# Kernel tuning notes

Measured on AMD Instinct MI355X. Metric: run time of the kernel, lower is better.

The kernel has to match this reference:

```python
import jax, jax.numpy as jnp
import numpy as np

ALPHA = 300.0  # attractor strength (exp variant: exp(-alpha*|dx|^gamma)*dx, gamma=2)


def setup_inputs() -> dict:
    key = jax.random.key(0)
    k0, k1, k2, k3 = jax.random.split(key, 4)
    n, c, h, w = 4, 256, 128, 128
    mlp_dim, n_attractors, n_bins = 128, 16, 64
    x = jax.random.normal(k0, (n, c, h, w), jnp.float32)
    b_prev = jax.random.uniform(k1, (n, n_bins, h, w), jnp.float32)  # bin centers
    w1 = jax.random.normal(k2, (mlp_dim, c), jnp.float32) * 0.02
    b1 = jnp.zeros((mlp_dim,), jnp.float32)
    w2 = jax.random.normal(k3, (n_attractors, mlp_dim), jnp.float32) * 0.02
    b2 = jnp.zeros((n_attractors,), jnp.float32)
    return {"x": x, "b_prev": b_prev, "w1": w1, "b1": b1, "w2": w2, "b2": b2}


def reference(x, b_prev, w1, b1, w2, b2):
    # 1x1 conv MLP head: Conv2d(c->mlp) -> ReLU -> Conv2d(mlp->n_attractors) -> Softplus
    hfeat = jax.nn.relu(jnp.einsum('nchw,oc->nohw', x, w1) + b1[None, :, None, None])
    A = jax.nn.softplus(jnp.einsum('nchw,oc->nohw', hfeat, w2) + b2[None, :, None, None])
    # b_prev interpolated to (h, w) == identity here (same spatial size)
    b_centers = b_prev
    # dx: [n, n_attractors, n_bins, h, w]
    dx = A[:, :, None, :, :] - b_centers[:, None, :, :, :]
    # exp attractor with gamma=2: exp(-alpha*dx^2) * dx, summed over attractors ('sum' kind)
    delta_c = jnp.sum(jnp.exp(-ALPHA * dx * dx) * dx, axis=1)
    b_new_centers = b_centers + delta_c
    return (b_new_centers, b_new_centers)
```

## Files before the change

kernel.cpp:

```cpp
#include <hip/hip_runtime.h>
#include <hip/hip_bf16.h>
#include <stdint.h>


#define HW 16384
#define ALPHA 300.0f

typedef short bf16x8_t __attribute__((ext_vector_type(8)));
typedef float f32x4_t __attribute__((ext_vector_type(4)));

__device__ __forceinline__ unsigned short f2bf(float f) {
  unsigned int u = __builtin_bit_cast(unsigned int, f);
  u += 0x7fffu + ((u >> 16) & 1u);
  return (unsigned short)(u >> 16);
}
__device__ __forceinline__ unsigned int pack2(float a, float b) {
  return (unsigned int)f2bf(a) | ((unsigned int)f2bf(b) << 16);
}

__global__ void zoed_prep(const float* __restrict__ w1,
                          const float* __restrict__ w2,
                          unsigned short* __restrict__ blob) {
  int i = blockIdx.x * 256 + threadIdx.x;
  if (i < 32768) {
    int o = i >> 8, c = i & 255;
    blob[(c >> 5) * 4096 + o * 32 + (c & 31)] = f2bf(w1[i]);
  } else {
    int i2 = i - 32768;
    int a = i2 >> 7, o = i2 & 127;
    blob[32768 + (o >> 5) * 512 + a * 32 + (o & 31)] = f2bf(w2[i2]);
  }
}

__global__ __launch_bounds__(256, 4) void zoed_mlp(
    const float* __restrict__ x, const float* __restrict__ b1,
    const float* __restrict__ b2, const unsigned short* __restrict__ wblob,
    float* __restrict__ A) {
  __shared__ __align__(16) char smem[16384];
  const int t = threadIdx.x;
  const int lane = t & 63;
  const int l15 = lane & 15;
  const int quad = lane >> 4;
  const int wv = t >> 6;
  char* hb = smem + wv * 4096;

  const int wid = blockIdx.x * 4 + wv;
  const int px0 = wid * 16;
  const int n = px0 >> 14;
  const int p = px0 & 16383;

  const float* xb = x + (size_t)(n * 256 + quad * 8) * HW + p + l15;
  float xr[8][8];
#pragma unroll
  for (int kc = 0; kc < 8; kc++)
#pragma unroll
    for (int j = 0; j < 8; j++) xr[kc][j] = xb[(size_t)(kc * 32 + j) * HW];

  f32x4_t acc[8];
#pragma unroll
  for (int m = 0; m < 8; m++) acc[m] = (f32x4_t){0.f, 0.f, 0.f, 0.f};

  const char* wb1 = (const char*)wblob + l15 * 64 + quad * 16;
#pragma unroll
  for (int kc = 0; kc < 8; kc++) {
    bf16x8_t bfrag;
    unsigned int* bu = (unsigned int*)&bfrag;
    bu[0] = pack2(xr[kc][0], xr[kc][1]);
    bu[1] = pack2(xr[kc][2], xr[kc][3]);
    bu[2] = pack2(xr[kc][4], xr[kc][5]);
    bu[3] = pack2(xr[kc][6], xr[kc][7]);
#pragma unroll
    for (int m = 0; m < 8; m++) {
      bf16x8_t af = *(const bf16x8_t*)(wb1 + kc * 8192 + m * 1024);
      acc[m] = __builtin_amdgcn_mfma_f32_16x16x32_bf16(af, bfrag, acc[m], 0, 0, 0);
    }
  }

#pragma unroll
  for (int m = 0; m < 8; m++) {
    f32x4_t b1v = *(const f32x4_t*)(b1 + m * 16 + quad * 4);
    f32x4_t h = acc[m] + b1v;
    h[0] = fmaxf(h[0], 0.f);
    h[1] = fmaxf(h[1], 0.f);
    h[2] = fmaxf(h[2], 0.f);
    h[3] = fmaxf(h[3], 0.f);
    int G = m * 2 + (quad >> 1);
    unsigned int* dst = (unsigned int*)(hb + l15 * 256 + ((G ^ (l15 & 3)) << 4) +
                                        (quad & 1) * 8);
    dst[0] = pack2(h[0], h[1]);
    dst[1] = pack2(h[2], h[3]);
  }

  f32x4_t acc2 = (f32x4_t){0.f, 0.f, 0.f, 0.f};
  const char* wb2 = (const char*)wblob + 65536 + l15 * 64 + quad * 16;
#pragma unroll
  for (int kc2 = 0; kc2 < 4; kc2++) {
    bf16x8_t a2 = *(const bf16x8_t*)(wb2 + kc2 * 1024);
    int G = kc2 * 4 + quad;
    bf16x8_t bh = *(const bf16x8_t*)(hb + l15 * 256 + ((G ^ (l15 & 3)) << 4));
    acc2 = __builtin_amdgcn_mfma_f32_16x16x32_bf16(a2, bh, acc2, 0, 0, 0);
  }
  f32x4_t b2v = *(const f32x4_t*)(b2 + quad * 4);
  float* Ab = A + (size_t)(n * 16 + quad * 4) * HW + p + l15;
#pragma unroll
  for (int r = 0; r < 4; r++) {
    float zz = acc2[r] + b2v[r];
    float sp = fmaxf(zz, 0.f) + log1pf(__expf(-fabsf(zz)));
    Ab[(size_t)r * HW] = sp;
  }
}

__global__ __launch_bounds__(256, 4) void zoed_attr(
    const float* __restrict__ bprev, const float* __restrict__ A,
    float* __restrict__ out) {
  const int t = threadIdx.x;
  const int blk = blockIdx.x;
  const int P = (blk & 255) * 256 + t;
  const int bg = blk >> 8;
  const int n = P >> 14;
  const int p = P & 16383;

  const float* Ab = A + (size_t)(n * 16) * HW + p;
  float Av[16];
#pragma unroll
  for (int a = 0; a < 16; a++) Av[a] = Ab[(size_t)a * HW];

  size_t obase = (size_t)(n * 64 + bg * 16) * HW + p;
  const float* bp = bprev + obase;
  float bpr[16];
#pragma unroll
  for (int b = 0; b < 16; b++) bpr[b] = bp[(size_t)b * HW];

  float* o1 = out + obase;
  float* o2 = out + (size_t)(4 * 64) * HW + obase;
#pragma unroll
  for (int b = 0; b < 16; b++) {
    float c = bpr[b];
    float d0 = 0.f, d1 = 0.f;
#pragma unroll
    for (int a = 0; a < 8; a++) {
      float dx = Av[a] - c;
      float e = __expf(dx * dx * -ALPHA);
      d0 = fmaf(e, dx, d0);
    }
#pragma unroll
    for (int a = 8; a < 16; a++) {
      float dx = Av[a] - c;
      float e = __expf(dx * dx * -ALPHA);
      d1 = fmaf(e, dx, d1);
    }
    float r = c + (d0 + d1);
    __builtin_nontemporal_store(r, o1 + (size_t)b * HW);
    __builtin_nontemporal_store(r, o2 + (size_t)b * HW);
  }
}

extern "C" void kernel_launch(void* const* d_in, const int* in_sizes, int n_in,
                              void* d_out, int out_size, void* d_ws,
                              size_t ws_size, hipStream_t stream) {
  const float* x = (const float*)d_in[0];
  const float* bprev = (const float*)d_in[1];
  const float* w1 = (const float*)d_in[2];
  const float* b1 = (const float*)d_in[3];
  const float* w2 = (const float*)d_in[4];
  const float* b2 = (const float*)d_in[5];
  float* outp = (float*)d_out;

  unsigned short* blob = (unsigned short*)d_ws;
  float* Abuf = (float*)((char*)d_ws + (1 << 20));

  zoed_prep<<<136, 256, 0, stream>>>(w1, w2, blob);
  zoed_mlp<<<1024, 256, 0, stream>>>(x, b1, b2, blob, Abuf);
  zoed_attr<<<1024, 256, 0, stream>>>(bprev, Abuf, outp);
}
```

Measured before the change: 156.7 us.

## Stream x tiles into LDS via async global_load_lds with ring-buffered prefetch

```diff
diff --git a/kernel.cpp b/kernel.cpp
--- a/kernel.cpp
+++ b/kernel.cpp
@@ -8,6 +8,10 @@
 
 typedef short bf16x8_t __attribute__((ext_vector_type(8)));
 typedef float f32x4_t __attribute__((ext_vector_type(4)));
+
+#define WAIT_VM(N) \
+  __builtin_amdgcn_s_waitcnt(((N)&0xF) | 0x70 | 0xF00 | (((N) >> 4) << 14))
+#define SB() __builtin_amdgcn_sched_barrier(0)
 
 __device__ __forceinline__ unsigned short f2bf(float f) {
   unsigned int u = __builtin_bit_cast(unsigned int, f);
@@ -16,6 +20,11 @@
 }
 __device__ __forceinline__ unsigned int pack2(float a, float b) {
   return (unsigned int)f2bf(a) | ((unsigned int)f2bf(b) << 16);
+}
+__device__ __forceinline__ void lds_dma16(const float* g, char* l) {
+  __builtin_amdgcn_global_load_lds(
+      (const __attribute__((address_space(1))) unsigned int*)g,
+      (__attribute__((address_space(3))) unsigned int*)l, 16, 0, 0);
 }
 
 __global__ void zoed_prep(const float* __restrict__ w1,
@@ -32,50 +41,81 @@
   }
 }
 
+template <int KC, int WN>
+__device__ __forceinline__ void g1_step(const char* xl, const char* wb1,
+                                        const float* xg, char* wbase,
+                                        f32x4_t (&acc)[8]) {
+  WAIT_VM(WN);
+  SB();
+  const char* xs = xl + (KC & 3) * 2048;
+  float xv[8];
+#pragma unroll
+  for (int j = 0; j < 8; j++) xv[j] = *(const float*)(xs + j * 64);
+  bf16x8_t bfrag;
+  unsigned int* bu = (unsigned int*)&bfrag;
+  bu[0] = pack2(xv[0], xv[1]);
+  bu[1] = pack2(xv[2], xv[3]);
+  bu[2] = pack2(xv[4], xv[5]);
+  bu[3] = pack2(xv[6], xv[7]);
+  SB();
+  if constexpr (KC < 4) {
+    lds_dma16(xg + (size_t)((KC + 4) * 32) * HW, wbase + (KC & 3) * 2048);
+    lds_dma16(xg + (size_t)((KC + 4) * 32 + 16) * HW,
+              wbase + (KC & 3) * 2048 + 1024);
+  }
+  bf16x8_t af[8];
+#pragma unroll
+  for (int m = 0; m < 8; m++)
+    af[m] = *(const bf16x8_t*)(wb1 + KC * 8192 + m * 1024);
+  SB();
+#pragma unroll
+  for (int m = 0; m < 8; m++)
+    acc[m] = __builtin_amdgcn_mfma_f32_16x16x32_bf16(af[m], bfrag, acc[m],
+                                                     0, 0, 0);
+}
+
 __global__ __launch_bounds__(256, 4) void zoed_mlp(
     const float* __restrict__ x, const float* __restrict__ b1,
     const float* __restrict__ b2, const unsigned short* __restrict__ wblob,
     float* __restrict__ A) {
-  __shared__ __align__(16) char smem[16384];
+  __shared__ __align__(16) char smem[32768];
   const int t = threadIdx.x;
   const int lane = t & 63;
   const int l15 = lane & 15;
   const int quad = lane >> 4;
   const int wv = t >> 6;
-  char* hb = smem + wv * 4096;
+  char* wbase = smem + wv * 8192;
 
   const int wid = blockIdx.x * 4 + wv;
-  const int px0 = wid * 16;
-  const int n = px0 >> 14;
-  const int p = px0 & 16383;
-
-  const float* xb = x + (size_t)(n * 256 + quad * 8) * HW + p + l15;
-  float xr[8][8];
-#pragma unroll
-  for (int kc = 0; kc < 8; kc++)
-#pragma unroll
-    for (int j = 0; j < 8; j++) xr[kc][j] = xb[(size_t)(kc * 32 + j) * HW];
+  const int n = wid >> 10;
+  const int p = (wid << 4) & 16383;
+
+  const float* xg =
+      x + (size_t)(n * 256 + (lane >> 2)) * HW + p + (lane & 3) * 4;
+
+#pragma unroll
+  for (int kc = 0; kc < 4; kc++) {
+    lds_dma16(xg + (size_t)(kc * 32) * HW, wbase + kc * 2048);
+    lds_dma16(xg + (size_t)(kc * 32 + 16) * HW, wbase + kc * 2048 + 1024);
+  }
 
   f32x4_t acc[8];
 #pragma unroll
   for (int m = 0; m < 8; m++) acc[m] = (f32x4_t){0.f, 0.f, 0.f, 0.f};
 
   const char* wb1 = (const char*)wblob + l15 * 64 + quad * 16;
-#pragma unroll
-  for (int kc = 0; kc < 8; kc++) {
-    bf16x8_t bfrag;
-    unsigned int* bu = (unsigned int*)&bfrag;
-    bu[0] = pack2(xr[kc][0], xr[kc][1]);
-    bu[1] = pack2(xr[kc][2], xr[kc][3]);
-    bu[2] = pack2(xr[kc][4], xr[kc][5]);
-    bu[3] = pack2(xr[kc][6], xr[kc][7]);
-#pragma unroll
-    for (int m = 0; m < 8; m++) {
-      bf16x8_t af = *(const bf16x8_t*)(wb1 + kc * 8192 + m * 1024);
-      acc[m] = __builtin_amdgcn_mfma_f32_16x16x32_bf16(af, bfrag, acc[m], 0, 0, 0);
-    }
-  }
-
+  const char* xl = wbase + (quad >> 1) * 1024 + (quad & 1) * 512 + l15 * 4;
+
+  g1_step<0, 6>(xl, wb1, xg, wbase, acc);
+  g1_step<1, 14>(xl, wb1, xg, wbase, acc);
+  g1_step<2, 22>(xl, wb1, xg, wbase, acc);
+  g1_step<3, 30>(xl, wb1, xg, wbase, acc);
+  g1_step<4, 38>(xl, wb1, xg, wbase, acc);
+  g1_step<5, 36>(xl, wb1, xg, wbase, acc);
+  g1_step<6, 34>(xl, wb1, xg, wbase, acc);
+  g1_step<7, 32>(xl, wb1, xg, wbase, acc);
+
+  char* hb = wbase;
 #pragma unroll
   for (int m = 0; m < 8; m++) {
     f32x4_t b1v = *(const f32x4_t*)(b1 + m * 16 + quad * 4);
@@ -85,8 +125,8 @@
     h[2] = fmaxf(h[2], 0.f);
     h[3] = fmaxf(h[3], 0.f);
     int G = m * 2 + (quad >> 1);
-    unsigned int* dst = (unsigned int*)(hb + l15 * 256 + ((G ^ (l15 & 3)) << 4) +
-                                        (quad & 1) * 8);
+    unsigned int* dst = (unsigned int*)(hb + l15 * 256 +
+                                        ((G ^ (l15 & 3)) << 4) + (quad & 1) * 8);
     dst[0] = pack2(h[0], h[1]);
     dst[1] = pack2(h[2], h[3]);
   }
```

Result: faster. 147.4 us (-6.0%).
